# Kernel optimization log

Measured on AMD Instinct MI355X. Metric: run time of the kernel, lower is better.

## Reference

```python
import jax, jax.numpy as jnp
import numpy as np

V, E, H, K, B, T = 32000, 512, 1024, 64, 64, 512


def setup_inputs() -> dict:
    key = jax.random.key(0)
    ks = jax.random.split(key, 12)
    nrm = lambda k, shape, sc: jax.random.normal(k, shape, jnp.float32) * sc
    inv_sqrt_h = 1.0 / np.sqrt(H)
    return {
        "x": jax.random.randint(ks[0], (B, T), 0, V),
        "tags": jax.random.randint(ks[1], (B, T), 0, K),
        "emb": nrm(ks[2], (V, E), 0.02),
        "w_ih": nrm(ks[3], (3 * H, E), inv_sqrt_h),
        "w_hh": nrm(ks[4], (3 * H, H), inv_sqrt_h),
        "b_ih": nrm(ks[5], (3 * H,), 0.01),
        "b_hh": nrm(ks[6], (3 * H,), 0.01),
        "fc_w": nrm(ks[7], (K, H), inv_sqrt_h),
        "fc_b": jnp.zeros((K,), jnp.float32),
        "start_trans": nrm(ks[8], (K,), 0.1),
        "end_trans": nrm(ks[9], (K,), 0.1),
        "trans": nrm(ks[10], (K, K), 0.1),
    }


def gru_scan(x_seq, w_ih, w_hh, b_ih, b_hh):
    # x_seq: [T, B, E] -> hidden states [T, B, H]; torch nn.GRU equations.
    Bn = x_seq.shape[1]
    Hd = w_hh.shape[1]
    # precompute input projections for all steps: [T, B, 3H]
    gi = jnp.einsum('tbe,ge->tbg', x_seq, w_ih) + b_ih

    def step(h, gi_t):
        gh = h @ w_hh.T + b_hh                      # [B, 3H]
        i_r, i_z, i_n = jnp.split(gi_t, 3, axis=-1)
        h_r, h_z, h_n = jnp.split(gh, 3, axis=-1)
        r = jax.nn.sigmoid(i_r + h_r)
        z = jax.nn.sigmoid(i_z + h_z)
        n = jnp.tanh(i_n + r * h_n)
        h_new = (1.0 - z) * n + z * h
        return h_new, h_new

    h0 = jnp.zeros((Bn, Hd), x_seq.dtype)
    _, hs = jax.lax.scan(step, h0, gi)
    return hs


def crf_nll(emissions, tags, start, end, trans):
    # emissions [B, T, K], tags [B, T]; torchcrf CRF, mask=None, reduction='sum'.
    em_t = jnp.swapaxes(emissions, 0, 1)   # [T, B, K]
    tg_t = jnp.swapaxes(tags, 0, 1)        # [T, B]
    Bn = emissions.shape[0]
    bidx = jnp.arange(Bn)

    # numerator: score of the gold path
    num0 = start[tg_t[0]] + em_t[0, bidx, tg_t[0]]

    def num_step(acc, xs):
        em_i, tag_prev, tag_cur = xs
        acc = acc + trans[tag_prev, tag_cur] + em_i[bidx, tag_cur]
        return acc, None

    num, _ = jax.lax.scan(num_step, num0, (em_t[1:], tg_t[:-1], tg_t[1:]))
    num = num + end[tg_t[-1]]

    # denominator: forward algorithm (log partition)
    alpha0 = start + em_t[0]                # [B, K]

    def den_step(alpha, em_i):
        # alpha[b,i] + trans[i,j] + em_i[b,j] -> logsumexp over i
        nxt = jax.scipy.special.logsumexp(
            alpha[:, :, None] + trans[None, :, :] + em_i[:, None, :], axis=1)
        return nxt, None

    alpha, _ = jax.lax.scan(den_step, alpha0, em_t[1:])
    den = jax.scipy.special.logsumexp(alpha + end, axis=1)
    return jnp.sum(den - num)  # = -sum(log-likelihood) = model's returned loss


def reference(x, tags, emb, w_ih, w_hh, b_ih, b_hh, fc_w, fc_b,
              start_trans, end_trans, trans):
    xe = emb[x]                              # [B, T, E]
    hs = gru_scan(jnp.swapaxes(xe, 0, 1), w_ih, w_hh, b_ih, b_hh)  # [T, B, H]
    gru_out = jnp.swapaxes(hs, 0, 1)         # [B, T, H]
    emissions = gru_out @ fc_w.T + fc_b      # [B, T, K]
    return crf_nll(emissions, tags, start_trans, end_trans, trans)
```

## Files before the change

### kernel.cpp

```cpp
#include <hip/hip_runtime.h>

typedef unsigned short USH;
typedef unsigned int u32;
typedef unsigned long long u64;
typedef float v4f __attribute__((ext_vector_type(4)));
typedef __bf16 v8bf __attribute__((ext_vector_type(8)));
typedef u32 v4u __attribute__((ext_vector_type(4)));

#define B_ 64
#define T_ 512
#define E_ 512
#define H_ 1024
#define NSCAN 128
#define EMIT0 128
#define NEMIT 111
#define CRF0  239
#define FINB  255

__device__ __forceinline__ USH f2b(float x) {
  union { float f; u32 u; } v; v.f = x;
  u32 r = v.u + 0x7FFFu + ((v.u >> 16) & 1u);
  return (USH)(r >> 16);
}
__device__ __forceinline__ v8bf pack8(float4 a, float4 b) {
  union { USH s[8]; v8bf v; } r;
  r.s[0] = f2b(a.x); r.s[1] = f2b(a.y); r.s[2] = f2b(a.z); r.s[3] = f2b(a.w);
  r.s[4] = f2b(b.x); r.s[5] = f2b(b.y); r.s[6] = f2b(b.z); r.s[7] = f2b(b.w);
  return r.v;
}
__device__ __forceinline__ v4f MF(v8bf a, v8bf b, v4f c) {
  return __builtin_amdgcn_mfma_f32_16x16x32_bf16(a, b, c, 0, 0, 0);
}
__device__ __forceinline__ float sigm(float x) { return 1.0f / (1.0f + __expf(-x)); }
__device__ __forceinline__ float tanhx(float x) { return 1.0f - 2.0f / (__expf(2.0f * x) + 1.0f); }

__device__ __forceinline__ v4u ldc16(u64 a) {
  v4u d;
  asm volatile("global_load_dwordx4 %0, %1, off sc0 sc1" : "=v"(d) : "v"(a));
  return d;
}
__device__ __forceinline__ void stc16(u64 a, v4u d) {
  asm volatile("global_store_dwordx4 %0, %1, off sc1" :: "v"(a), "v"(d) : "memory");
}
__device__ __forceinline__ void stdw(u64 a, u32 v) {
  asm volatile("global_store_dword %0, %1, off sc1" :: "v"(a), "v"(v) : "memory");
}

__global__ void gatherk(const int* __restrict__ x, const float* __restrict__ emb, USH* __restrict__ xeb) {
  int r = blockIdx.x;
  int id = x[r];
  const float4* e = reinterpret_cast<const float4*>(emb + (long)id * E_);
  float4 v = e[threadIdx.x];
  ushort4 q = make_ushort4(f2b(v.x), f2b(v.y), f2b(v.z), f2b(v.w));
  *reinterpret_cast<ushort4*>(xeb + (long)r * E_ + threadIdx.x * 4) = q;
}

__global__ __launch_bounds__(256, 1) void fused(
    const USH* __restrict__ xeb, const float* __restrict__ wih, const float* __restrict__ whh,
    const float* __restrict__ bih, const float* __restrict__ bhh, char* __restrict__ hsC,
    const float* __restrict__ fcw, const float* __restrict__ fcb,
    float* __restrict__ em, const int* __restrict__ tags, const float* __restrict__ stv,
    const float* __restrict__ env, const float* __restrict__ trn, float* __restrict__ res,
    float* __restrict__ outp)
{
  __shared__ float redS[6144];
  __shared__ USH  trpS[512];

  const int tid = threadIdx.x;
  const int wv = tid >> 6, ln = tid & 63;
  const int l16 = ln & 15, lq = ln >> 4;
  const v4f z4 = {0.f, 0.f, 0.f, 0.f};

  if (blockIdx.x < NSCAN) {
    const int bg = blockIdx.x >> 6, cb = blockIdx.x & 63;
    const int b0 = bg * 32, c0 = cb * 16;

    v8bf wihf[4][3], whhf[8][3];
    #pragma unroll
    for (int kt = 0; kt < 4; ++kt)
      #pragma unroll
      for (int g = 0; g < 3; ++g) {
        const float* wp = wih + (size_t)(g * H_ + c0 + l16) * E_ + (wv * 16 + kt * 4 + lq) * 8;
        wihf[kt][g] = pack8(*reinterpret_cast<const float4*>(wp),
                            *reinterpret_cast<const float4*>(wp + 4));
      }
    #pragma unroll
    for (int kt = 0; kt < 8; ++kt)
      #pragma unroll
      for (int g = 0; g < 3; ++g) {
        const float* wp = whh + (size_t)(g * H_ + c0 + l16) * H_ + (wv * 32 + kt * 4 + lq) * 8;
        whhf[kt][g] = pack8(*reinterpret_cast<const float4*>(wp),
                            *reinterpret_cast<const float4*>(wp + 4));
      }

    const int cgl = c0 + l16;
    const float bir = bih[cgl], biz = bih[H_ + cgl], bin = bih[2 * H_ + cgl];
    const float bhr = bhh[cgl], bhz = bhh[H_ + cgl], bhn = bhh[2 * H_ + cgl];

    const USH* a1b = xeb + (size_t)(b0 + l16) * (T_ * E_) + wv * 128 + 8 * lq;
    const u64 hC = (u64)(uintptr_t)hsC + (u64)bg * 65536;
    const int lane_off = (wv * 16 + (lq >> 1)) * 1024 + l16 * 32 + (lq & 1) * 16;
    const u64 probe_off = (u64)((wv * 16 + l16) * 1024 + 1020);

    float hp0 = 0.f, hp1 = 0.f, hp2 = 0.f, hp3 = 0.f;
    v4f* rv = reinterpret_cast<v4f*>(redS);

    uint4 pf[8];
    #pragma unroll
    for (int kt = 0; kt < 4; ++kt) {
      pf[kt * 2]     = *reinterpret_cast<const uint4*>(a1b + kt * 32);
      pf[kt * 2 + 1] = *reinterpret_cast<const uint4*>(a1b + 16 * (T_ * E_) + kt * 32);
    }
    u32 pr = 0;

    for (int t = 0; t < T_; ++t) {
      v4f acc[8];
      #pragma unroll
      for (int i = 0; i < 8; ++i) acc[i] = z4;

      #pragma unroll
      for (int kt = 0; kt < 4; ++kt) {
        v8bf a0 = __builtin_bit_cast(v8bf, pf[kt * 2]);
        v8bf a1f = __builtin_bit_cast(v8bf, pf[kt * 2 + 1]);
        acc[0] = MF(a0, wihf[kt][0], acc[0]); acc[1] = MF(a1f, wihf[kt][0], acc[1]);
        acc[2] = MF(a0, wihf[kt][1], acc[2]); acc[3] = MF(a1f, wihf[kt][1], acc[3]);
        acc[4] = MF(a0, wihf[kt][2], acc[4]); acc[5] = MF(a1f, wihf[kt][2], acc[5]);
      }

      if (t > 0) {
        const u64 hbase = hC + (u64)(t - 1) * 131072;
        while (true) {
          asm volatile("s_waitcnt vmcnt(0)" ::: "memory");
          __builtin_amdgcn_sched_barrier(0);
          if (__ballot(pr != 0xFFFFFFFFu) == ~0ull) break;
          asm volatile("global_load_dword %0, %1, off sc0 sc1" : "=v"(pr) : "v"(hbase + probe_off));
        }
        v4u ha[16];
        while (true) {
          #pragma unroll
          for (int kt = 0; kt < 8; ++kt) {
            ha[kt * 2]     = ldc16(hbase + lane_off + kt * 2048);
            ha[kt * 2 + 1] = ldc16(hbase + lane_off + kt * 2048 + 512);
          }
          asm volatile("s_waitcnt vmcnt(0)" ::: "memory");
          __builtin_amdgcn_sched_barrier(0);
          bool bad = false;
          #pragma unroll
          for (int f = 0; f < 16; ++f) {
            #pragma unroll
            for (int d = 0; d < 4; ++d) bad |= (ha[f][d] == 0xFFFFFFFFu);
          }
          if (__ballot(bad) == 0ull) break;
          __builtin_amdgcn_s_sleep(1);
        }
        #pragma unroll
        for (int kt = 0; kt < 8; ++kt) {
          v8bf a0 = __builtin_bit_cast(v8bf, ha[kt * 2]);
          v8bf a1f = __builtin_bit_cast(v8bf, ha[kt * 2 + 1]);
          acc[0] = MF(a0, whhf[kt][0], acc[0]); acc[1] = MF(a1f, whhf[kt][0], acc[1]);
          acc[2] = MF(a0, whhf[kt][1], acc[2]); acc[3] = MF(a1f, whhf[kt][1], acc[3]);
          acc[6] = MF(a0, whhf[kt][2], acc[6]); acc[7] = MF(a1f, whhf[kt][2], acc[7]);
        }
      }

      if (wv >= 2) {
        #pragma unroll
        for (int f = 0; f < 8; ++f) rv[(wv - 2) * 512 + f * 64 + ln] = acc[f];
      } else if (wv == 0) {
        #pragma unroll
        for (int j = 0; j < 4; ++j) rv[1024 + j * 64 + ln] = acc[2 * j + 1];
      } else {
        #pragma unroll
        for (int j = 0; j < 4; ++j) rv[1280 + j * 64 + ln] = acc[2 * j];
      }
      __syncthreads();

      if (wv < 2) {
        v4f m0, m1, m2, m3;
        if (wv == 0) {
          m0 = acc[0]; m1 = acc[2]; m2 = acc[4]; m3 = acc[6];
          #pragma unroll
          for (int w = 0; w < 2; ++w) {
            m0 += rv[w * 512 + 0 * 64 + ln]; m1 += rv[w * 512 + 2 * 64 + ln];
            m2 += rv[w * 512 + 4 * 64 + ln]; m3 += rv[w * 512 + 6 * 64 + ln];
          }
          m0 += rv[1280 + 0 * 64 + ln]; m1 += rv[1280 + 1 * 64 + ln];
          m2 += rv[1280 + 2 * 64 + ln]; m3 += rv[1280 + 3 * 64 + ln];
        } else {
          m0 = acc[1]; m1 = acc[3]; m2 = acc[5]; m3 = acc[7];
          #pragma unroll
          for (int w = 0; w < 2; ++w) {
            m0 += rv[w * 512 + 1 * 64 + ln]; m1 += rv[w * 512 + 3 * 64 + ln];
            m2 += rv[w * 512 + 5 * 64 + ln]; m3 += rv[w * 512 + 7 * 64 + ln];
          }
          m0 += rv[1024 + 0 * 64 + ln]; m1 += rv[1024 + 1 * 64 + ln];
          m2 += rv[1024 + 2 * 64 + ln]; m3 += rv[1024 + 3 * 64 + ln];
        }
        #pragma unroll
        for (int r4 = 0; r4 < 4; ++r4) {
          float rg = sigm(m0[r4] + bir + bhr);
          float zg = sigm(m1[r4] + biz + bhz);
          float ng = tanhx(m2[r4] + bin + rg * (m3[r4] + bhn));
          float hprev = (r4 == 0 ? hp0 : r4 == 1 ? hp1 : r4 == 2 ? hp2 : hp3);
          float hn = (1.f - zg) * ng + zg * hprev;
          if (r4 == 0) hp0 = hn; else if (r4 == 1) hp1 = hn; else if (r4 == 2) hp2 = hn; else hp3 = hn;
          trpS[(wv * 16 + lq * 4 + r4) * 16 + l16] = f2b(hn);
        }
        if (ln < 32) {
          v4u hv = *reinterpret_cast<const v4u*>(trpS + wv * 256 + ln * 8);
          stc16(hC + (u64)t * 131072 + (u64)cb * 1024 + (u64)(wv * 512) + (u64)ln * 16, hv);
        }
      }

      {
        const u64 hb = hC + (u64)t * 131072;
        asm volatile("global_load_dword %0, %1, off sc0 sc1" : "=v"(pr) : "v"(hb + probe_off));
        const USH* a1n = a1b + (size_t)(t + 1 < T_ ? t + 1 : t) * E_;
        #pragma unroll
        for (int kt = 0; kt < 4; ++kt) {
          pf[kt * 2]     = *reinterpret_cast<const uint4*>(a1n + kt * 32);
          pf[kt * 2 + 1] = *reinterpret_cast<const uint4*>(a1n + 16 * (T_ * E_) + kt * 32);
        }
      }
    }
  } else if (blockIdx.x < CRF0) {
    const int e = blockIdx.x - EMIT0;
    v8bf fcf[8][4];
    #pragma unroll
    for (int kt = 0; kt < 8; ++kt)
      #pragma unroll
      for (int nt = 0; nt < 4; ++nt) {
        const float* wp = fcw + (size_t)(nt * 16 + l16) * H_ + wv * 256 + kt * 32 + lq * 8;
        fcf[kt][nt] = pack8(*reinterpret_cast<const float4*>(wp),
                            *reinterpret_cast<const float4*>(wp + 4));
      }
    float bias[4];
    #pragma unroll
    for (int nt = 0; nt < 4; ++nt) bias[nt] = fcb[nt * 16 + l16];

    v4f* rvE = reinterpret_cast<v4f*>(redS);
    for (int tile = e; tile < 2048; tile += NEMIT) {
      int t = tile >> 2, bq = tile & 3;
      const u64 ab = (u64)(uintptr_t)hsC + (u64)t * 131072 + (u64)(bq >> 1) * 65536
                   + (u64)((bq & 1) * 16 + l16) * 32 + (u64)(wv * 16 + (lq >> 1)) * 1024 + (u64)(lq & 1) * 16;
      v4u ha2[8];
      while (true) {
        #pragma unroll
        for (int kt = 0; kt < 8; ++kt) ha2[kt] = ldc16(ab + kt * 2048);
        asm volatile("s_waitcnt vmcnt(0)" ::: "memory");
        __builtin_amdgcn_sched_barrier(0);
        bool bad = false;
        #pragma unroll
        for (int kt = 0; kt < 8; ++kt) {
          #pragma unroll
          for (int d = 0; d < 4; ++d) bad |= (ha2[kt][d] == 0xFFFFFFFFu);
        }
        if (__ballot(bad) == 0ull) break;
        __builtin_amdgcn_s_sleep(32);
      }
      v4f acc[4];
      #pragma unroll
      for (int nt = 0; nt < 4; ++nt) acc[nt] = z4;
      #pragma unroll
      for (int kt = 0; kt < 8; ++kt) {
        v8bf a = __builtin_bit_cast(v8bf, ha2[kt]);
        #pragma unroll
        for (int nt = 0; nt < 4; ++nt) acc[nt] = MF(a, fcf[kt][nt], acc[nt]);
      }
      __syncthreads();
      if (wv != 0) {
        #pragma unroll
        for (int nt = 0; nt < 4; ++nt) rvE[(wv - 1) * 256 + nt * 64 + ln] = acc[nt];
      }
      __syncthreads();
      if (wv == 0) {
        #pragma unroll
        for (int nt = 0; nt < 4; ++nt) {
          v4f s = acc[nt];
          #pragma unroll
          for (int w = 0; w < 3; ++w) s += rvE[w * 256 + nt * 64 + ln];
          int k = nt * 16 + l16;
          #pragma unroll
          for (int r = 0; r < 4; ++r) {
            int b = bq * 16 + lq * 4 + r;
            float val = s[r] + bias[nt];
            u32 vb; { union { float f; u32 u; } c; c.f = val; vb = c.u; }
            u64 ea = (u64)(uintptr_t)em + ((((size_t)b * T_ + t) * 64) + k) * 4;
            stdw(ea, vb);
          }
        }
      }
    }
  } else if (blockIdx.x < FINB) {
    float* trsS = redS;
    int* tgS = (int*)(redS + 4096);
    for (int i = tid; i < 4096; i += 256) trsS[i] = trn[i];
    const int b = (blockIdx.x - CRF0) * 4 + wv;
    for (int i = ln; i < T_; i += 64) tgS[wv * 512 + i] = tags[b * T_ + i];
    __syncthreads();
    const int j = ln;
    const float stj = stv[j], enj = env[j];
    const u64 emb0 = (u64)(uintptr_t)em + ((size_t)b * T_) * 256 + (size_t)j * 4;
    float alpha = 0.f, num = 0.f; int tprev = 0;
    for (int t = 0; t < T_; ++t) {
      u32 ev;
      const u64 ea = emb0 + (size_t)t * 256;
      while (true) {
        asm volatile("global_load_dword %0, %1, off sc0 sc1" : "=v"(ev) : "v"(ea));
        asm volatile("s_waitcnt vmcnt(0)" ::: "memory");
        __builtin_amdgcn_sched_barrier(0);
        if (__ballot(ev == 0xFFFFFFFFu) == 0ull) break;
        __builtin_amdgcn_s_sleep(16);
      }
      float e; { union { u32 u; float f; } c; c.u = ev; e = c.f; }
      int ct = tgS[wv * 512 + t];
      float esh = __shfl(e, ct, 64);
      if (t == 0) {
        alpha = stj + e;
        num = stv[ct] + esh;
      } else {
        num += trsS[tprev * 64 + ct] + esh;
        float vv[64];
        #pragma unroll
        for (int i = 0; i < 64; ++i) vv[i] = __shfl(alpha, i, 64) + trsS[i * 64 + j];
        float mc[4];
        #pragma unroll
        for (int c4 = 0; c4 < 4; ++c4) {
          mc[c4] = vv[c4 * 16];
          #pragma unroll
          for (int ii = 1; ii < 16; ++ii) mc[c4] = fmaxf(mc[c4], vv[c4 * 16 + ii]);
        }
        float M = fmaxf(fmaxf(mc[0], mc[1]), fmaxf(mc[2], mc[3]));
        float sc[4] = {0.f, 0.f, 0.f, 0.f};
        #pragma unroll
        for (int c4 = 0; c4 < 4; ++c4)
          #pragma unroll
          for (int ii = 0; ii < 16; ++ii) sc[c4] += __expf(vv[c4 * 16 + ii] - M);
        alpha = M + __logf((sc[0] + sc[1]) + (sc[2] + sc[3])) + e;
      }
      tprev = ct;
    }
    num += env[tprev];
    float v = alpha + enj;
    float mm = v;
    #pragma unroll
    for (int o = 32; o; o >>= 1) mm = fmaxf(mm, __shfl_xor(mm, o, 64));
    float ss = __expf(v - mm);
    #pragma unroll
    for (int o = 32; o; o >>= 1) ss += __shfl_xor(ss, o, 64);
    if (j == 0) {
      float r = (mm + __logf(ss)) - num;
      u32 rb; { union { float f; u32 u; } c; c.f = r; rb = c.u; }
      stdw((u64)(uintptr_t)res + (size_t)b * 4, rb);
    }
  } else {
    if (tid < 64) {
      u32 rb;
      const u64 ra = (u64)(uintptr_t)res + (size_t)tid * 4;
      while (true) {
        asm volatile("global_load_dword %0, %1, off sc0 sc1" : "=v"(rb) : "v"(ra));
        asm volatile("s_waitcnt vmcnt(0)" ::: "memory");
        __builtin_amdgcn_sched_barrier(0);
        if (__ballot(rb == 0xFFFFFFFFu) == 0ull) break;
        __builtin_amdgcn_s_sleep(32);
      }
      float v; { union { u32 u; float f; } c; c.u = rb; v = c.f; }
      #pragma unroll
      for (int o = 32; o; o >>= 1) v += __shfl_xor(v, o, 64);
      if (tid == 0) outp[0] = v;
    }
  }
}

extern "C" void kernel_launch(void* const* d_in, const int* in_sizes, int n_in,
                              void* d_out, int out_size, void* d_ws, size_t ws_size,
                              hipStream_t stream) {
  (void)in_sizes; (void)n_in; (void)out_size;
  const int*   x    = (const int*)d_in[0];
  const int*   tags = (const int*)d_in[1];
  const float* emb  = (const float*)d_in[2];
  const float* wih  = (const float*)d_in[3];
  const float* whh  = (const float*)d_in[4];
  const float* bih  = (const float*)d_in[5];
  const float* bhh  = (const float*)d_in[6];
  const float* fcw  = (const float*)d_in[7];
  const float* fcb  = (const float*)d_in[8];
  const float* str  = (const float*)d_in[9];
  const float* enr  = (const float*)d_in[10];
  const float* trn  = (const float*)d_in[11];

  char* ws = (char*)d_ws;
  char*  hsC  = ws;
  float* em   = (float*)(ws + 67108864);
  float* res  = (float*)(ws + 75497472);
  USH*   xeb  = (USH*)(ws + 75497728);
  if (ws_size < 109052160ull) return;

  hipMemsetAsync(ws, 0xFF, 75497728ull, stream);

  gatherk<<<B_ * T_, 128, 0, stream>>>(x, emb, xeb);
  fused<<<256, 256, 0, stream>>>(xeb, wih, whh, bih, bhh, hsC, fcw, fcb,
                                 em, tags, str, enr, trn, res, (float*)d_out);
}
```

Baseline: 2.166 ms.

## Use 512-thread blocks with two column halves per scan block, halving grid

Moves the fused persistent kernel from 256-thread blocks to 512-thread blocks. Each GRU scan block now covers 32 hidden columns with two 4-wave halves, so there are 64 scan blocks instead of 128. Emission blocks run two sub-streams each, and CRF blocks handle 8 batch rows each. The aim is fewer blocks polling the cross-block flag handshake each step, and fewer participants to synchronise per timestep. The cost is more work and more shared memory per block, and block-wide __syncthreads now spans both halves.

Result: slower. 4.227 ms (+95.1%).

```diff
diff --git a/kernel.cpp b/kernel.cpp
--- a/kernel.cpp
+++ b/kernel.cpp
@@ -11,11 +11,11 @@
 #define T_ 512
 #define E_ 512
 #define H_ 1024
-#define NSCAN 128
-#define EMIT0 128
-#define NEMIT 111
-#define CRF0  239
-#define FINB  255
+#define NSCAN 64
+#define EMIT0 64
+#define CRF0  128
+#define FINB  136
+#define GRID  137
 
 __device__ __forceinline__ USH f2b(float x) {
   union { float f; u32 u; } v; v.f = x;
@@ -55,7 +55,7 @@
   *reinterpret_cast<ushort4*>(xeb + (long)r * E_ + threadIdx.x * 4) = q;
 }
 
-__global__ __launch_bounds__(256, 1) void fused(
+__global__ __launch_bounds__(512, 1) void fused(
     const USH* __restrict__ xeb, const float* __restrict__ wih, const float* __restrict__ whh,
     const float* __restrict__ bih, const float* __restrict__ bhh, char* __restrict__ hsC,
     const float* __restrict__ fcw, const float* __restrict__ fcb,
@@ -63,24 +63,25 @@
     const float* __restrict__ env, const float* __restrict__ trn, float* __restrict__ res,
     float* __restrict__ outp)
 {
-  __shared__ float redS[6144];
-  __shared__ USH  trpS[512];
+  __shared__ float redS[12288];
+  __shared__ USH  trpS[1024];
 
   const int tid = threadIdx.x;
-  const int wv = tid >> 6, ln = tid & 63;
-  const int l16 = ln & 15, lq = ln >> 4;
   const v4f z4 = {0.f, 0.f, 0.f, 0.f};
 
   if (blockIdx.x < NSCAN) {
-    const int bg = blockIdx.x >> 6, cb = blockIdx.x & 63;
-    const int b0 = bg * 32, c0 = cb * 16;
+    const int wv = tid >> 6, ln = tid & 63;
+    const int l16 = ln & 15, lq = ln >> 4;
+    const int half = wv >> 2, kq = wv & 3;
+    const int bg = blockIdx.x >> 5, cb = blockIdx.x & 31;
+    const int b0 = bg * 32, c0 = cb * 32;
 
     v8bf wihf[4][3], whhf[8][3];
     #pragma unroll
     for (int kt = 0; kt < 4; ++kt)
       #pragma unroll
       for (int g = 0; g < 3; ++g) {
-        const float* wp = wih + (size_t)(g * H_ + c0 + l16) * E_ + (wv * 16 + kt * 4 + lq) * 8;
+        const float* wp = wih + (size_t)(g * H_ + c0 + half * 16 + l16) * E_ + kq * 128 + kt * 32 + lq * 8;
         wihf[kt][g] = pack8(*reinterpret_cast<const float4*>(wp),
                             *reinterpret_cast<const float4*>(wp + 4));
       }
@@ -88,22 +89,23 @@
     for (int kt = 0; kt < 8; ++kt)
       #pragma unroll
       for (int g = 0; g < 3; ++g) {
-        const float* wp = whh + (size_t)(g * H_ + c0 + l16) * H_ + (wv * 32 + kt * 4 + lq) * 8;
+        const float* wp = whh + (size_t)(g * H_ + c0 + half * 16 + l16) * H_ + kq * 256 + kt * 32 + lq * 8;
         whhf[kt][g] = pack8(*reinterpret_cast<const float4*>(wp),
                             *reinterpret_cast<const float4*>(wp + 4));
       }
 
-    const int cgl = c0 + l16;
+    const int cgl = c0 + half * 16 + l16;
     const float bir = bih[cgl], biz = bih[H_ + cgl], bin = bih[2 * H_ + cgl];
     const float bhr = bhh[cgl], bhz = bhh[H_ + cgl], bhn = bhh[2 * H_ + cgl];
 
-    const USH* a1b = xeb + (size_t)(b0 + l16) * (T_ * E_) + wv * 128 + 8 * lq;
+    const USH* a1b = xeb + (size_t)(b0 + l16) * (T_ * E_) + kq * 128 + lq * 8;
     const u64 hC = (u64)(uintptr_t)hsC + (u64)bg * 65536;
-    const int lane_off = (wv * 16 + (lq >> 1)) * 1024 + l16 * 32 + (lq & 1) * 16;
-    const u64 probe_off = (u64)((wv * 16 + l16) * 1024 + 1020);
+    const int lane_off = (lq >> 1) * 1024 + l16 * 32 + (lq & 1) * 16;
+    const u64 probe_off = (u64)((kq * 8 + (ln & 7)) * 2048 + 2044);
 
     float hp0 = 0.f, hp1 = 0.f, hp2 = 0.f, hp3 = 0.f;
     v4f* rv = reinterpret_cast<v4f*>(redS);
+    const int rbase = half * 1536;
 
     uint4 pf[8];
     #pragma unroll
@@ -139,8 +141,8 @@
         while (true) {
           #pragma unroll
           for (int kt = 0; kt < 8; ++kt) {
-            ha[kt * 2]     = ldc16(hbase + lane_off + kt * 2048);
-            ha[kt * 2 + 1] = ldc16(hbase + lane_off + kt * 2048 + 512);
+            ha[kt * 2]     = ldc16(hbase + (u64)((kq * 8 + kt) * 2048) + lane_off);
+            ha[kt * 2 + 1] = ldc16(hbase + (u64)((kq * 8 + kt) * 2048 + 512) + lane_off);
           }
           asm volatile("s_waitcnt vmcnt(0)" ::: "memory");
           __builtin_amdgcn_sched_barrier(0);
@@ -163,38 +165,38 @@
         }
       }
 
-      if (wv >= 2) {
-        #pragma unroll
-        for (int f = 0; f < 8; ++f) rv[(wv - 2) * 512 + f * 64 + ln] = acc[f];
-      } else if (wv == 0) {
-        #pragma unroll
-        for (int j = 0; j < 4; ++j) rv[1024 + j * 64 + ln] = acc[2 * j + 1];
+      if (kq >= 2) {
+        #pragma unroll
+        for (int f = 0; f < 8; ++f) rv[rbase + (kq - 2) * 512 + f * 64 + ln] = acc[f];
+      } else if (kq == 0) {
+        #pragma unroll
+        for (int j = 0; j < 4; ++j) rv[rbase + 1024 + j * 64 + ln] = acc[2 * j + 1];
       } else {
         #pragma unroll
-        for (int j = 0; j < 4; ++j) rv[1280 + j * 64 + ln] = acc[2 * j];
+        for (int j = 0; j < 4; ++j) rv[rbase + 1280 + j * 64 + ln] = acc[2 * j];
       }
       __syncthreads();
 
-      if (wv < 2) {
+      if (kq < 2) {
         v4f m0, m1, m2, m3;
-        if (wv == 0) {
+        if (kq == 0) {
           m0 = acc[0]; m1 = acc[2]; m2 = acc[4]; m3 = acc[6];
           #pragma unroll
           for (int w = 0; w < 2; ++w) {
-            m0 += rv[w * 512 + 0 * 64 + ln]; m1 += rv[w * 512 + 2 * 64 + ln];
-            m2 += rv[w * 512 + 4 * 64 + ln]; m3 += rv[w * 512 + 6 * 64 + ln];
+            m0 += rv[rbase + w * 512 + 0 * 64 + ln]; m1 += rv[rbase + w * 512 + 2 * 64 + ln];
+            m2 += rv[rbase + w * 512 + 4 * 64 + ln]; m3 += rv[rbase + w * 512 + 6 * 64 + ln];
           }
-          m0 += rv[1280 + 0 * 64 + ln]; m1 += rv[1280 + 1 * 64 + ln];
-          m2 += rv[1280 + 2 * 64 + ln]; m3 += rv[1280 + 3 * 64 + ln];
+          m0 += rv[rbase + 1280 + 0 * 64 + ln]; m1 += rv[rbase + 1280 + 1 * 64 + ln];
+          m2 += rv[rbase + 1280 + 2 * 64 + ln]; m3 += rv[rbase + 1280 + 3 * 64 + ln];
         } else {
           m0 = acc[1]; m1 = acc[3]; m2 = acc[5]; m3 = acc[7];
           #pragma unroll
           for (int w = 0; w < 2; ++w) {
-            m0 += rv[w * 512 + 1 * 64 + ln]; m1 += rv[w * 512 + 3 * 64 + ln];
-            m2 += rv[w * 512 + 5 * 64 + ln]; m3 += rv[w * 512 + 7 * 64 + ln];
+            m0 += rv[rbase + w * 512 + 1 * 64 + ln]; m1 += rv[rbase + w * 512 + 3 * 64 + ln];
+            m2 += rv[rbase + w * 512 + 5 * 64 + ln]; m3 += rv[rbase + w * 512 + 7 * 64 + ln];
           }
-          m0 += rv[1024 + 0 * 64 + ln]; m1 += rv[1024 + 1 * 64 + ln];
-          m2 += rv[1024 + 2 * 64 + ln]; m3 += rv[1024 + 3 * 64 + ln];
+          m0 += rv[rbase + 1024 + 0 * 64 + ln]; m1 += rv[rbase + 1024 + 1 * 64 + ln];
+          m2 += rv[rbase + 1024 + 2 * 64 + ln]; m3 += rv[rbase + 1024 + 3 * 64 + ln];
         }
         #pragma unroll
         for (int r4 = 0; r4 < 4; ++r4) {
@@ -204,11 +206,12 @@
           float hprev = (r4 == 0 ? hp0 : r4 == 1 ? hp1 : r4 == 2 ? hp2 : hp3);
           float hn = (1.f - zg) * ng + zg * hprev;
           if (r4 == 0) hp0 = hn; else if (r4 == 1) hp1 = hn; else if (r4 == 2) hp2 = hn; else hp3 = hn;
-          trpS[(wv * 16 + lq * 4 + r4) * 16 + l16] = f2b(hn);
+          trpS[half * 512 + (kq * 16 + lq * 4 + r4) * 16 + l16] = f2b(hn);
         }
         if (ln < 32) {
-          v4u hv = *reinterpret_cast<const v4u*>(trpS + wv * 256 + ln * 8);
-          stc16(hC + (u64)t * 131072 + (u64)cb * 1024 + (u64)(wv * 512) + (u64)ln * 16, hv);
+          int off = half * 1024 + kq * 512 + (ln >> 1) * 32 + (ln & 1) * 16;
+          v4u hv = *reinterpret_cast<const v4u*>(reinterpret_cast<const char*>(trpS) + off);
+          stc16(hC + (u64)t * 131072 + (u64)(cb * 2048) + (u64)off, hv);
         }
       }
 
@@ -224,7 +227,9 @@
       }
     }
   } else if (blockIdx.x < CRF0) {
-    const int e = blockIdx.x - EMIT0;
+    const int sub = tid >> 8, stid = tid & 255;
+    const int wv = stid >> 6, ln = stid & 63, l16 = ln & 15, lq = ln >> 4;
+    const int stream = (blockIdx.x - EMIT0) * 2 + sub;
     v8bf fcf[8][4];
     #pragma unroll
     for (int kt = 0; kt < 8; ++kt)
@@ -238,15 +243,15 @@
     #pragma unroll
     for (int nt = 0; nt < 4; ++nt) bias[nt] = fcb[nt * 16 + l16];
 
-    v4f* rvE = reinterpret_cast<v4f*>(redS);
-    for (int tile = e; tile < 2048; tile += NEMIT) {
+    v4f* rvE = reinterpret_cast<v4f*>(redS) + sub * 768;
+    for (int tile = stream; tile < 2048; tile += 128) {
       int t = tile >> 2, bq = tile & 3;
       const u64 ab = (u64)(uintptr_t)hsC + (u64)t * 131072 + (u64)(bq >> 1) * 65536
-                   + (u64)((bq & 1) * 16 + l16) * 32 + (u64)(wv * 16 + (lq >> 1)) * 1024 + (u64)(lq & 1) * 16;
+                   + (u64)((lq >> 1) * 1024 + ((bq & 1) * 16 + l16) * 32 + (lq & 1) * 16);
       v4u ha2[8];
       while (true) {
         #pragma unroll
-        for (int kt = 0; kt < 8; ++kt) ha2[kt] = ldc16(ab + kt * 2048);
+        for (int kt = 0; kt < 8; ++kt) ha2[kt] = ldc16(ab + (u64)((wv * 8 + kt) * 2048));
         asm volatile("s_waitcnt vmcnt(0)" ::: "memory");
         __builtin_amdgcn_sched_barrier(0);
         bool bad = false;
@@ -285,17 +290,17 @@
             int b = bq * 16 + lq * 4 + r;
             float val = s[r] + bias[nt];
             u32 vb; { union { float f; u32 u; } c; c.f = val; vb = c.u; }
-            u64 ea = (u64)(uintptr_t)em + ((((size_t)b * T_ + t) * 64) + k) * 4;
-            stdw(ea, vb);
+            stdw((u64)(uintptr_t)em + ((((size_t)b * T_ + t) * 64) + k) * 4, vb);
           }
         }
       }
     }
   } else if (blockIdx.x < FINB) {
+    const int wv = tid >> 6, ln = tid & 63;
     float* trsS = redS;
     int* tgS = (int*)(redS + 4096);
-    for (int i = tid; i < 4096; i += 256) trsS[i] = trn[i];
-    const int b = (blockIdx.x - CRF0) * 4 + wv;
+    for (int i = tid; i < 4096; i += 512) trsS[i] = trn[i];
+    const int b = (blockIdx.x - CRF0) * 8 + wv;
     for (int i = ln; i < T_; i += 64) tgS[wv * 512 + i] = tags[b * T_ + i];
     __syncthreads();
     const int j = ln;
@@ -399,6 +404,6 @@
   hipMemsetAsync(ws, 0xFF, 75497728ull, stream);
 
   gatherk<<<B_ * T_, 128, 0, stream>>>(x, emb, xeb);
-  fused<<<256, 256, 0, stream>>>(xeb, wih, whh, bih, bhh, hsC, fcw, fcb,
-                                 em, tags, str, enr, trn, res, (float*)d_out);
-}
+  fused<<<GRID, 512, 0, stream>>>(xeb, wih, whh, bih, bhh, hsC, fcw, fcb,
+                                  em, tags, str, enr, trn, res, (float*)d_out);
+}
```
